# Kernel optimization log

Measured on AMD Instinct MI355X. Metric: run time of the kernel, lower is better.

## Reference

```python
import jax, jax.numpy as jnp
import numpy as np

V, D, N, DK, DV, H, DFF = 32000, 512, 6, 64, 64, 8, 2048
B, S = 8, 512
EPS = 1e-5


def _pe(seq_len, d_model):
    pos = np.arange(seq_len)[:, None].astype(np.float32)
    i = np.arange(0, d_model, 2).astype(np.float32)
    ang = pos / np.power(10000.0, i / d_model)
    pe = np.zeros((seq_len, d_model), dtype=np.float32)
    pe[:, 0::2] = np.sin(ang)
    pe[:, 1::2] = np.cos(ang)
    return jnp.asarray(pe)


def _ln(x, g, b):
    m = jnp.mean(x, axis=-1, keepdims=True)
    v = jnp.mean(jnp.square(x - m), axis=-1, keepdims=True)
    return (x - m) * jax.lax.rsqrt(v + EPS) * g + b


def _mha(xq, xkv, Wq, Wk, Wv, bq, bk, bv, mask):
    # Wq/Wk: [H,D,DK], Wv: [H,D,DV]; mask: [B,Sq,Skv] additive
    q = jnp.einsum('bsd,hdk->bhsk', xq, Wq) + bq[None, :, None, :]
    k = jnp.einsum('bsd,hdk->bhsk', xkv, Wk) + bk[None, :, None, :]
    v = jnp.einsum('bsd,hdk->bhsk', xkv, Wv) + bv[None, :, None, :]
    scores = jnp.einsum('bhqk,bhsk->bhqs', q, k) / jnp.sqrt(jnp.float32(DK))
    scores = scores + mask[:, None, :, :]
    attn = jax.nn.softmax(scores, axis=-1)
    out = jnp.einsum('bhqs,bhsv->bhqv', attn, v)  # [B,H,Sq,DV]
    return out.transpose(0, 2, 1, 3).reshape(xq.shape[0], xq.shape[1], H * DV)


def setup_inputs() -> dict:
    key = jax.random.key(0)
    ks = jax.random.split(key, 24)
    sc = 0.02
    inp = {
        'decoder_input': jax.random.randint(ks[0], (B, S), 0, V),
        'encoder_output': jax.random.normal(ks[1], (B, S, D), dtype=jnp.float32),
        'self_mask': jnp.where(jnp.tril(jnp.ones((S, S), dtype=bool)), 0.0, -1e9)[None].repeat(B, 0).astype(jnp.float32),
        'cross_mask': jnp.zeros((B, S, S), dtype=jnp.float32),
        'emb': jax.random.normal(ks[2], (V, D), dtype=jnp.float32),
        'Wq_s': jax.random.normal(ks[3], (N, H, D, DK)) * sc,
        'Wk_s': jax.random.normal(ks[4], (N, H, D, DK)) * sc,
        'Wv_s': jax.random.normal(ks[5], (N, H, D, DV)) * sc,
        'bq_s': jnp.zeros((N, H, DK)), 'bk_s': jnp.zeros((N, H, DK)), 'bv_s': jnp.zeros((N, H, DV)),
        'Wq_c': jax.random.normal(ks[6], (N, H, D, DK)) * sc,
        'Wk_c': jax.random.normal(ks[7], (N, H, D, DK)) * sc,
        'Wv_c': jax.random.normal(ks[8], (N, H, D, DV)) * sc,
        'bq_c': jnp.zeros((N, H, DK)), 'bk_c': jnp.zeros((N, H, DK)), 'bv_c': jnp.zeros((N, H, DV)),
        'W1': jax.random.normal(ks[9], (N, D, DFF)) * sc,
        'b1': jnp.zeros((N, DFF)),
        'W2': jax.random.normal(ks[10], (N, DFF, D)) * sc,
        'b2': jnp.zeros((N, D)),
        'ln1_g': jnp.ones((N, D)), 'ln1_b': jnp.zeros((N, D)),
        'ln2_g': jnp.ones((N, D)), 'ln2_b': jnp.zeros((N, D)),
    }
    return inp


def reference(decoder_input, encoder_output, self_mask, cross_mask, emb,
              Wq_s, Wk_s, Wv_s, bq_s, bk_s, bv_s,
              Wq_c, Wk_c, Wv_c, bq_c, bk_c, bv_c,
              W1, b1, W2, b2, ln1_g, ln1_b, ln2_g, ln2_b):
    x = emb[decoder_input] + _pe(decoder_input.shape[1], D)[None]
    for l in range(N):
        sa = _mha(x, x, Wq_s[l], Wk_s[l], Wv_s[l], bq_s[l], bk_s[l], bv_s[l], self_mask)
        x = _ln(x + sa, ln1_g[l], ln1_b[l])
        ca = _mha(x, encoder_output, Wq_c[l], Wk_c[l], Wv_c[l], bq_c[l], bk_c[l], bv_c[l], cross_mask)
        x = _ln(x + ca, ln2_g[l], ln2_b[l])
        ff = jax.nn.relu(jnp.einsum('bsd,df->bsf', x, W1[l]) + b1[l])
        ff = jnp.einsum('bsf,fd->bsd', ff, W2[l]) + b2[l]
        # source reuses layer_norm2 for the third norm (layer_norm3 is dead)
        x = _ln(x + ff, ln2_g[l], ln2_b[l])
    return x
```

## Files before the change

kernel.cpp:

```cpp
#include <hip/hip_runtime.h>
#include <hip/hip_bf16.h>
#include <math.h>

#define BB 8
#define SS 512
#define DDIM 512
#define HH 8
#define DFFV 2048
#define NLAYER 6
#define EPSV 1e-5f
#define WQS 0.180336880f

typedef __attribute__((ext_vector_type(8))) short bf16x8;
typedef __attribute__((ext_vector_type(4))) float f32x4;

static __device__ __forceinline__ ushort f2bf(float f) {
  union { float f; unsigned u; } uf; uf.f = f;
  unsigned u = uf.u;
  unsigned r = (u + 0x7fffu + ((u >> 16) & 1u)) >> 16;
  return (ushort)r;
}
static __device__ __forceinline__ float bf2f(ushort h) {
  union { unsigned u; float f; } x;
  x.u = ((unsigned)h) << 16;
  return x.f;
}

static __device__ __forceinline__ void gload_lds16(const void* g, void* l) {
  __builtin_amdgcn_global_load_lds(
      (const __attribute__((address_space(1))) void*)g,
      (__attribute__((address_space(3))) void*)l, 16, 0, 0);
}

__global__ __launch_bounds__(256) void prep_kernel(
    const int* __restrict__ idx, const float* __restrict__ emb,
    const float* __restrict__ enc, const float* __restrict__ bq,
    const float* __restrict__ bk, const float* __restrict__ bv,
    const float* __restrict__ bkc, const float* __restrict__ bvc,
    const float* __restrict__ bqc, ushort* __restrict__ xb,
    ushort* __restrict__ encb, float* __restrict__ qkvb,
    float* __restrict__ ckvb, float* __restrict__ cqb) {
  int gid = blockIdx.x * 256 + threadIdx.x;
  {
    int t0 = gid * 4;
    int bs = t0 >> 9;
    int s = bs & (SS - 1);
    int tok = idx[bs];
    ushort4 o;
    float vv[4];
#pragma unroll
    for (int e = 0; e < 4; e++) {
      int d = (t0 + e) & (DDIM - 1);
      int i2 = d & ~1;
      float ang = (float)s * powf(10000.0f, -((float)i2) / (float)DDIM);
      float pe = (d & 1) ? cosf(ang) : sinf(ang);
      vv[e] = emb[(size_t)tok * DDIM + d] + pe;
    }
    o.x = f2bf(vv[0]); o.y = f2bf(vv[1]); o.z = f2bf(vv[2]); o.w = f2bf(vv[3]);
    *reinterpret_cast<ushort4*>(xb + t0) = o;
  }
  {
    float4 v = reinterpret_cast<const float4*>(enc)[gid];
    ushort4 o;
    o.x = f2bf(v.x); o.y = f2bf(v.y); o.z = f2bf(v.z); o.w = f2bf(v.w);
    reinterpret_cast<ushort4*>(encb)[gid] = o;
  }
  int t = gid;
  if (t < NLAYER * 1536) {
    int l = t / 1536, n = t % 1536;
    float v = n < 512 ? bq[l * 512 + n] * WQS
                      : (n < 1024 ? bk[l * 512 + n - 512] : bv[l * 512 + n - 1024]);
    qkvb[t] = v;
  }
  if (t < NLAYER * 1024) {
    int l = t / 1024, n = t % 1024;
    ckvb[t] = n < 512 ? bkc[l * 512 + n] : bvc[l * 512 + n - 512];
  }
  if (t < NLAYER * 512) cqb[t] = bqc[t] * WQS;
}

__global__ __launch_bounds__(256) void wtrans_kernel(
    const float* __restrict__ in, ushort* __restrict__ out, int R, int C,
    int lgH, size_t zl, float scale) {
  __shared__ float t[32][33];
  int z = blockIdx.z;
  int l = z >> lgH, hh = z & ((1 << lgH) - 1);
  const float* ip = in + (size_t)z * R * C;
  ushort* op = out + (size_t)l * zl + (size_t)hh * R * C;
  int j = threadIdx.x & 31, i0 = threadIdx.x >> 5;
  int r0 = blockIdx.y * 32, c0 = blockIdx.x * 32;
#pragma unroll
  for (int p = 0; p < 4; p++) {
    int r = r0 + i0 + p * 8;
    t[i0 + p * 8][j] = ip[(size_t)r * C + c0 + j];
  }
  __syncthreads();
#pragma unroll
  for (int p = 0; p < 4; p++) {
    int cc = c0 + i0 + p * 8;
    op[(size_t)cc * R + r0 + j] = f2bf(t[j][i0 + p * 8] * scale);
  }
}

__global__ __launch_bounds__(256) void wtrans6_kernel(
    const float* __restrict__ qs, const float* __restrict__ ks,
    const float* __restrict__ vs, const float* __restrict__ qc,
    const float* __restrict__ kc, const float* __restrict__ vc,
    ushort* __restrict__ wqkv, ushort* __restrict__ wqc,
    ushort* __restrict__ wckv) {
  __shared__ float t[32][33];
  int z = blockIdx.z;
  int job = z / 48, zz = z % 48;
  const float* in; ushort* out; size_t zl; float scale;
  switch (job) {
    case 0: in = qs; out = wqkv;           zl = 786432; scale = WQS; break;
    case 1: in = ks; out = wqkv + 262144;  zl = 786432; scale = 1.f; break;
    case 2: in = vs; out = wqkv + 524288;  zl = 786432; scale = 1.f; break;
    case 3: in = qc; out = wqc;            zl = 262144; scale = WQS; break;
    case 4: in = kc; out = wckv;           zl = 524288; scale = 1.f; break;
    default: in = vc; out = wckv + 262144; zl = 524288; scale = 1.f; break;
  }
  int l = zz >> 3, hh = zz & 7;
  const float* ip = in + (size_t)zz * 512 * 64;
  ushort* op = out + (size_t)l * zl + (size_t)hh * 512 * 64;
  int j = threadIdx.x & 31, i0 = threadIdx.x >> 5;
  int r0 = blockIdx.y * 32, c0 = blockIdx.x * 32;
#pragma unroll
  for (int p = 0; p < 4; p++) {
    int r = r0 + i0 + p * 8;
    t[i0 + p * 8][j] = ip[(size_t)r * 64 + c0 + j];
  }
  __syncthreads();
#pragma unroll
  for (int p = 0; p < 4; p++) {
    int cc = c0 + i0 + p * 8;
    op[(size_t)cc * 512 + r0 + j] = f2bf(t[j][i0 + p * 8] * scale);
  }
}

template <int BM, int BN, int RELU, int OUTBF, int NTV, int LGP, int SPLITK,
          int SWZ>
__global__ __launch_bounds__(256) void gemm_mfma(
    const ushort* __restrict__ A, const ushort* __restrict__ Bw,
    const float* __restrict__ bias, float* __restrict__ Cf,
    ushort* __restrict__ Cb, ushort* __restrict__ vt, int M, int N, int K) {
  constexpr int WM = BM / 64;
  constexpr int WN = 4 / WM;
  constexpr int W = BN / WN;
  constexpr int AF = 4;
  constexpr int BF = W / 16;
  constexpr int GA = BM * 8;
  constexpr int GPT = (BM + BN) * 8 / 256;
  __shared__ __align__(16) ushort lds_s[2][(BM + BN) * 64];
  int bn, bm;
  if (SWZ) {
    int nwg = gridDim.x * gridDim.y;
    int wg = blockIdx.y * gridDim.x + blockIdx.x;
    int cpx = nwg >> 3;
    int swz = (wg & 7) * cpx + (wg >> 3);
    bn = (swz % gridDim.x) * BN;
    bm = (swz / gridDim.x) * BM;
  } else {
    bn = blockIdx.x * BN;
    bm = blockIdx.y * BM;
  }
  int kz = (SPLITK > 1) ? blockIdx.z : 0;
  int Keff = K / SPLITK;
  int kbase = kz * Keff;
  int tid = threadIdx.x, lane = tid & 63, w = tid >> 6;
  int wm = w / WN, wn = w % WN;
  int c = lane & 15, g16 = lane >> 4;
  f32x4 acc[AF][BF] = {};

  auto STAGE = [&](int k0, int bufi) {
#pragma unroll
    for (int i = 0; i < GPT; i++) {
      int gidx = i * 256 + tid;
      int gbase = (i * 4 + w) * 64;
      const ushort* src;
      if (gidx < GA) {
        int row = gidx >> 3, dg = gidx & 7;
        src = A + (size_t)(bm + row) * K + kbase + k0 + ((dg ^ (row & 7)) << 3);
      } else {
        int bidx = gidx - GA;
        int row = bidx >> 3, dg = bidx & 7;
        src = Bw + (size_t)(bn + row) * K + kbase + k0 + ((dg ^ (row & 7)) << 3);
      }
      gload_lds16(src, (void*)((char*)(&lds_s[bufi][0]) + gbase * 16));
    }
  };

  int nk = Keff >> 6;
  STAGE(0, 0);
  for (int kt = 0; kt < nk; kt++) {
    int cur = kt & 1;
    if (kt + 1 < nk) {
      STAGE((kt + 1) << 6, cur ^ 1);
      asm volatile("s_waitcnt vmcnt(%0)" ::"n"(GPT) : "memory");
    } else {
      asm volatile("s_waitcnt vmcnt(0)" ::: "memory");
    }
    __builtin_amdgcn_s_barrier();
    __builtin_amdgcn_sched_barrier(0);
    const ushort* Alds = &lds_s[cur][0];
    const ushort* Blds = &lds_s[cur][BM * 64];
#pragma unroll
    for (int ks = 0; ks < 2; ks++) {
      int g = ks * 4 + g16;
      bf16x8 a[AF], b[BF];
#pragma unroll
      for (int i = 0; i < AF; i++) {
        int R = wm * 64 + i * 16 + c;
        a[i] = *(const bf16x8*)(Alds + R * 64 + ((g ^ (R & 7)) << 3));
      }
#pragma unroll
      for (int j = 0; j < BF; j++) {
        int Rb = wn * W + j * 16 + c;
        b[j] = *(const bf16x8*)(Blds + Rb * 64 + ((g ^ (Rb & 7)) << 3));
      }
#pragma unroll
      for (int i = 0; i < AF; i++)
#pragma unroll
        for (int j = 0; j < BF; j++)
          acc[i][j] = __builtin_amdgcn_mfma_f32_16x16x32_bf16(a[i], b[j],
                                                              acc[i][j], 0, 0, 0);
    }
    __builtin_amdgcn_sched_barrier(0);
    __builtin_amdgcn_s_barrier();
  }
  int rb = g16 * 4;
#pragma unroll
  for (int j = 0; j < BF; j++) {
    int col = bn + wn * W + j * 16 + c;
    float bv = (SPLITK > 1 && kz != 0) ? 0.0f : bias[col];
    int cc = LGP ? (col & ((1 << LGP) - 1)) : col;
    int lp = LGP ? (col >> LGP) : 0;
    if (NTV > 0 && cc >= NTV) {
      int hh = (cc - NTV) >> 6, dv = col & 63;
      ushort* vtl = vt + (size_t)lp * 2097152;
#pragma unroll
      for (int i = 0; i < AF; i++) {
        int row = bm + wm * 64 + i * 16 + rb;
        int b_ = row >> 9, s_ = row & 511;
        ushort4 o4;
        o4.x = f2bf(acc[i][j][0] + bv);
        o4.y = f2bf(acc[i][j][1] + bv);
        o4.z = f2bf(acc[i][j][2] + bv);
        o4.w = f2bf(acc[i][j][3] + bv);
        *reinterpret_cast<ushort4*>(
            vtl + ((size_t)(b_ * 8 + hh) * 64 + dv) * 512 + s_) = o4;
      }
    } else {
#pragma unroll
      for (int i = 0; i < AF; i++) {
#pragma unroll
        for (int qq = 0; qq < 4; qq++) {
          int row = bm + wm * 64 + i * 16 + rb + qq;
          float v = acc[i][j][qq] + bv;
          if (RELU) v = fmaxf(v, 0.0f);
          if (OUTBF)
            Cb[(size_t)row * N + col] = f2bf(v);
          else
            Cf[(size_t)kz * M * N + (size_t)row * N + col] = v;
        }
      }
    }
  }
}

template <int MASKED, int NW>
__global__ __launch_bounds__(NW * 64) void attn_mfma(
    const ushort* __restrict__ q, int qstr, const ushort* __restrict__ k,
    int kstr, const ushort* __restrict__ vt, ushort* __restrict__ out) {
  __shared__ __align__(16) char lds[32768 + NW * 2048];
  int h = blockIdx.y, b = blockIdx.z;
  int qc = blockIdx.x;
  if (MASKED && (b & 4)) qc = gridDim.x - 1 - qc;
  int q0 = qc * (NW * 16);
  int tid = threadIdx.x, lane = tid & 63, w = tid >> 6;
  int c = lane & 15, g16 = lane >> 4, rb = g16 * 4;

  bf16x8 qa[2];
#pragma unroll
  for (int ks = 0; ks < 2; ks++)
    qa[ks] = *(const bf16x8*)(q + (size_t)(b * SS + q0 + 16 * w + c) * qstr +
                              h * 64 + ks * 32 + g16 * 8);
  f32x4 o[4] = {};
  float mq = -1e30f, lq = 0.f;

  int nt = MASKED ? (q0 >> 6) + 1 : 8;
  int pbase = 32768 + w * 2048;

  constexpr int GPTK = 512 / (NW * 64);
  bf16x8 rk[GPTK], rv[GPTK];
  const ushort* vbase = vt + ((size_t)(b * 8 + h) * 64) * 512;
  auto LOADT = [&](int kv0) {
#pragma unroll
    for (int i = 0; i < GPTK; i++) {
      int idx = tid + i * (NW * 64);
      int row = idx >> 3, gw = idx & 7;
      rk[i] = *(const bf16x8*)(k + (size_t)(b * SS + kv0 + row) * kstr +
                               h * 64 + gw * 8);
      rv[i] = *(const bf16x8*)(vbase + (size_t)row * 512 + kv0 + gw * 8);
    }
  };
  auto WRT = [&](int bufi) {
    char* p = lds + bufi * 16384;
#pragma unroll
    for (int i = 0; i < GPTK; i++) {
      int idx = tid + i * (NW * 64);
      int row = idx >> 3, gw = idx & 7;
      *(bf16x8*)(p + row * 128 + ((gw ^ (row & 7)) << 4)) = rk[i];
      *(bf16x8*)(p + 8192 + row * 128 + ((gw ^ (row & 7)) << 4)) = rv[i];
    }
  };
  LOADT(0);
  WRT(0);
  for (int t = 0; t < nt; t++) {
    if (t + 1 < nt) LOADT((t + 1) * 64);
    __syncthreads();
    char* kb_ = lds + (t & 1) * 16384;
    char* vb_ = kb_ + 8192;
    f32x4 sp[4] = {};
    __builtin_amdgcn_s_setprio(1);
#pragma unroll
    for (int ks = 0; ks < 2; ks++) {
      int g = ks * 4 + g16;
#pragma unroll
      for (int f = 0; f < 4; f++) {
        int row = f * 16 + c;
        bf16x8 k8 = *(bf16x8*)(kb_ + row * 128 + ((g ^ (row & 7)) << 4));
        sp[f] = __builtin_amdgcn_mfma_f32_16x16x32_bf16(k8, qa[ks], sp[f], 0, 0, 0);
      }
    }
    __builtin_amdgcn_s_setprio(0);
    if (MASKED && t == nt - 1) {
      int ql = 16 * w + c;
#pragma unroll
      for (int f = 0; f < 4; f++)
#pragma unroll
        for (int j = 0; j < 4; j++)
          sp[f][j] += (f * 16 + rb + j) <= ql ? 0.0f : -1e9f;
    }
    float tmax = -1e30f;
#pragma unroll
    for (int f = 0; f < 4; f++)
#pragma unroll
      for (int j = 0; j < 4; j++) tmax = fmaxf(tmax, sp[f][j]);
    tmax = fmaxf(tmax, __shfl_xor(tmax, 16));
    tmax = fmaxf(tmax, __shfl_xor(tmax, 32));
    if (!__all(tmax <= mq + 4.0f)) {
      float mn = fmaxf(mq, tmax);
      float scq = exp2f(mq - mn);
      mq = mn;
      lq *= scq;
      int sb = lane & 48;
#pragma unroll
      for (int j = 0; j < 4; j++) {
        float scj = __shfl(scq, sb | (rb + j));
        o[0][j] *= scj; o[1][j] *= scj; o[2][j] *= scj; o[3][j] *= scj;
      }
    }
    float psum = 0.f;
#pragma unroll
    for (int f = 0; f < 4; f++)
#pragma unroll
      for (int j = 0; j < 4; j++) {
        float pv = exp2f(sp[f][j] - mq);
        sp[f][j] = pv;
        psum += pv;
      }
    psum += __shfl_xor(psum, 16);
    psum += __shfl_xor(psum, 32);
    lq += psum;
#pragma unroll
    for (int f = 0; f < 4; f++) {
      int kv0 = f * 16 + rb;
      ushort4 pk;
      pk.x = f2bf(sp[f][0]); pk.y = f2bf(sp[f][1]);
      pk.z = f2bf(sp[f][2]); pk.w = f2bf(sp[f][3]);
      int gg = kv0 >> 3, off = (kv0 & 7) * 2;
      *(ushort4*)(lds + pbase + c * 128 + ((gg ^ (c & 7)) << 4) + off) = pk;
    }
    __builtin_amdgcn_s_setprio(1);
#pragma unroll
    for (int ks2 = 0; ks2 < 2; ks2++) {
      int g = ks2 * 4 + g16;
      bf16x8 pa = *(bf16x8*)(lds + pbase + c * 128 + ((g ^ (c & 7)) << 4));
#pragma unroll
      for (int f = 0; f < 4; f++) {
        int row = f * 16 + c;
        bf16x8 v8 = *(bf16x8*)(vb_ + row * 128 + ((g ^ (row & 7)) << 4));
        o[f] = __builtin_amdgcn_mfma_f32_16x16x32_bf16(pa, v8, o[f], 0, 0, 0);
      }
    }
    __builtin_amdgcn_s_setprio(0);
    if (t + 1 < nt) WRT((t + 1) & 1);
  }
  float invq = 1.0f / lq;
  int sb = lane & 48;
#pragma unroll
  for (int j = 0; j < 4; j++) {
    float invj = __shfl(invq, sb | (rb + j));
    size_t rowo = (size_t)(b * SS + q0 + 16 * w + rb + j) * 512 + h * 64;
#pragma unroll
    for (int f = 0; f < 4; f++)
      out[rowo + f * 16 + c] = f2bf(o[f][j] * invj);
  }
}

template <int Y2>
__global__ __launch_bounds__(256) void add_ln_kernel(
    ushort* __restrict__ xb, const ushort* __restrict__ yb,
    const float* __restrict__ y0, const float* __restrict__ y1,
    const float* __restrict__ g, const float* __restrict__ bta,
    float* __restrict__ xf) {
  int row = blockIdx.x * 4 + (threadIdx.x >> 6);
  int lane = threadIdx.x & 63;
  int base = row * DDIM + lane * 8;
  bf16x8 xv = *reinterpret_cast<const bf16x8*>(xb + base);
  float v[8];
  if (Y2) {
    float4 a0 = *reinterpret_cast<const float4*>(y0 + base);
    float4 a1 = *reinterpret_cast<const float4*>(y0 + base + 4);
    float4 c0 = *reinterpret_cast<const float4*>(y1 + base);
    float4 c1 = *reinterpret_cast<const float4*>(y1 + base + 4);
    v[0] = bf2f((ushort)xv[0]) + a0.x + c0.x;
    v[1] = bf2f((ushort)xv[1]) + a0.y + c0.y;
    v[2] = bf2f((ushort)xv[2]) + a0.z + c0.z;
    v[3] = bf2f((ushort)xv[3]) + a0.w + c0.w;
    v[4] = bf2f((ushort)xv[4]) + a1.x + c1.x;
    v[5] = bf2f((ushort)xv[5]) + a1.y + c1.y;
    v[6] = bf2f((ushort)xv[6]) + a1.z + c1.z;
    v[7] = bf2f((ushort)xv[7]) + a1.w + c1.w;
  } else {
    bf16x8 yv = *reinterpret_cast<const bf16x8*>(yb + base);
#pragma unroll
    for (int i = 0; i < 8; i++)
      v[i] = bf2f((ushort)xv[i]) + bf2f((ushort)yv[i]);
  }
  float s = 0.f;
#pragma unroll
  for (int i = 0; i < 8; i++) s += v[i];
#pragma unroll
  for (int off = 32; off > 0; off >>= 1) s += __shfl_xor(s, off);
  float mean = s * (1.0f / DDIM);
  float t2 = 0.f;
#pragma unroll
  for (int i = 0; i < 8; i++) {
    v[i] -= mean;
    t2 += v[i] * v[i];
  }
#pragma unroll
  for (int off = 32; off > 0; off >>= 1) t2 += __shfl_xor(t2, off);
  float rs = rsqrtf(t2 * (1.0f / DDIM) + EPSV);
  int cidx = lane * 8;
  float4 g0 = *reinterpret_cast<const float4*>(g + cidx);
  float4 g1 = *reinterpret_cast<const float4*>(g + cidx + 4);
  float4 b0 = *reinterpret_cast<const float4*>(bta + cidx);
  float4 b1 = *reinterpret_cast<const float4*>(bta + cidx + 4);
  float o[8];
  o[0] = v[0] * rs * g0.x + b0.x; o[1] = v[1] * rs * g0.y + b0.y;
  o[2] = v[2] * rs * g0.z + b0.z; o[3] = v[3] * rs * g0.w + b0.w;
  o[4] = v[4] * rs * g1.x + b1.x; o[5] = v[5] * rs * g1.y + b1.y;
  o[6] = v[6] * rs * g1.z + b1.z; o[7] = v[7] * rs * g1.w + b1.w;
  bf16x8 ob;
#pragma unroll
  for (int i = 0; i < 8; i++) ob[i] = (short)f2bf(o[i]);
  *reinterpret_cast<bf16x8*>(xb + base) = ob;
  if (xf) {
    float4 w0 = {o[0], o[1], o[2], o[3]}, w1 = {o[4], o[5], o[6], o[7]};
    *reinterpret_cast<float4*>(xf + base) = w0;
    *reinterpret_cast<float4*>(xf + base + 4) = w1;
  }
}

extern "C" void kernel_launch(void* const* d_in, const int* in_sizes, int n_in,
                              void* d_out, int out_size, void* d_ws,
                              size_t ws_size, hipStream_t stream) {
  const int* dec = (const int*)d_in[0];
  const float* enc = (const float*)d_in[1];
  const float* emb = (const float*)d_in[4];
  const float* Wq_s = (const float*)d_in[5];
  const float* Wk_s = (const float*)d_in[6];
  const float* Wv_s = (const float*)d_in[7];
  const float* bq_s = (const float*)d_in[8];
  const float* bk_s = (const float*)d_in[9];
  const float* bv_s = (const float*)d_in[10];
  const float* Wq_c = (const float*)d_in[11];
  const float* Wk_c = (const float*)d_in[12];
  const float* Wv_c = (const float*)d_in[13];
  const float* bq_c = (const float*)d_in[14];
  const float* bk_c = (const float*)d_in[15];
  const float* bv_c = (const float*)d_in[16];
  const float* W1 = (const float*)d_in[17];
  const float* b1 = (const float*)d_in[18];
  const float* W2 = (const float*)d_in[19];
  const float* b2 = (const float*)d_in[20];
  const float* ln1_g = (const float*)d_in[21];
  const float* ln1_b = (const float*)d_in[22];
  const float* ln2_g = (const float*)d_in[23];
  const float* ln2_b = (const float*)d_in[24];

  char* ws = (char*)d_ws;
  ushort* wqkv = (ushort*)(ws + 0);
  ushort* wqc = (ushort*)(ws + 9437184ull);
  ushort* wckv = (ushort*)(ws + 12582912ull);
  ushort* w1t = (ushort*)(ws + 18874368ull);
  ushort* w2t = (ushort*)(ws + 31457280ull);
  ushort* encb = (ushort*)(ws + 44040192ull);
  ushort* xb = (ushort*)(ws + 48234496ull);
  ushort* tmpb = (ushort*)(ws + 52428800ull);
  float* tmpf = (float*)(ws + 56623104ull);
  ushort* qkvbuf = (ushort*)(ws + 73400320ull);
  ushort* cq = (ushort*)(ws + 73400320ull);
  ushort* ff1b = (ushort*)(ws + 73400320ull);
  ushort* vt = (ushort*)(ws + 85983232ull);
  float* qkvbias = (float*)(ws + 90177536ull);
  float* ckvbias = (float*)(ws + 90214400ull);
  ushort* ckvbuf = (ushort*)(ws + 90238976ull);
  ushort* vtc = (ushort*)(ws + 140570624ull);
  float* cqbias = (float*)(ws + 165736448ull);

  const int M = BB * SS;
  dim3 g256(256);

  prep_kernel<<<dim3(2048), g256, 0, stream>>>(dec, emb, enc, bq_s, bk_s, bv_s,
                                               bk_c, bv_c, bq_c, xb, encb,
                                               qkvbias, ckvbias, cqbias);
  wtrans6_kernel<<<dim3(2, 16, 288), g256, 0, stream>>>(
      Wq_s, Wk_s, Wv_s, Wq_c, Wk_c, Wv_c, wqkv, wqc, wckv);
  wtrans_kernel<<<dim3(64, 16, 6), g256, 0, stream>>>(W1, w1t, 512, 2048, 0,
                                                      1048576ull, 1.0f);
  wtrans_kernel<<<dim3(16, 64, 6), g256, 0, stream>>>(W2, w2t, 2048, 512, 0,
                                                      1048576ull, 1.0f);

  gemm_mfma<128, 128, 0, 1, 512, 10, 1, 0><<<dim3(48, 32), g256, 0, stream>>>(
      encb, wckv, ckvbias, nullptr, ckvbuf, vtc, M, 6144, 512);

  for (int l = 0; l < NLAYER; l++) {
    gemm_mfma<64, 128, 0, 1, 1024, 0, 1, 1><<<dim3(12, 64), g256, 0, stream>>>(
        xb, wqkv + (size_t)l * 786432, qkvbias + l * 1536, nullptr, qkvbuf, vt,
        M, 1536, 512);
    attn_mfma<1, 4><<<dim3(8, 8, 8), g256, 0, stream>>>(
        qkvbuf, 1536, qkvbuf + 512, 1536, vt, tmpb);
    add_ln_kernel<0><<<dim3(M / 4), g256, 0, stream>>>(
        xb, tmpb, nullptr, nullptr, ln1_g + l * 512, ln1_b + l * 512, nullptr);
    gemm_mfma<64, 128, 0, 1, 0, 0, 1, 1><<<dim3(4, 64), g256, 0, stream>>>(
        xb, wqc + (size_t)l * 262144, cqbias + l * 512, nullptr, cq, nullptr,
        M, 512, 512);
    attn_mfma<0, 8><<<dim3(4, 8, 8), dim3(512), 0, stream>>>(
        cq, 512, ckvbuf + l * 1024, 6144, vtc + (size_t)l * 2097152, tmpb);
    add_ln_kernel<0><<<dim3(M / 4), g256, 0, stream>>>(
        xb, tmpb, nullptr, nullptr, ln2_g + l * 512, ln2_b + l * 512, nullptr);
    gemm_mfma<64, 128, 1, 1, 0, 0, 1, 1><<<dim3(16, 64), g256, 0, stream>>>(
        xb, w1t + (size_t)l * 1048576, b1 + l * DFFV, nullptr, ff1b, nullptr,
        M, DFFV, 512);
    gemm_mfma<64, 128, 0, 0, 0, 0, 2, 1><<<dim3(4, 64, 2), g256, 0, stream>>>(
        ff1b, w2t + (size_t)l * 1048576, b2 + l * 512, tmpf, nullptr, nullptr,
        M, 512, DFFV);
    add_ln_kernel<1><<<dim3(M / 4), g256, 0, stream>>>(
        xb, nullptr, tmpf, tmpf + (size_t)M * 512, ln2_g + l * 512,
        ln2_b + l * 512, (l == NLAYER - 1) ? (float*)d_out : nullptr);
  }
}
```

Measured before the change: 621.5 us.

## Fuse cross-attention Q projection into the attention kernel

```diff
diff --git a/kernel.cpp b/kernel.cpp
--- a/kernel.cpp
+++ b/kernel.cpp
@@ -268,10 +268,11 @@
   }
 }
 
-template <int MASKED, int NW>
+template <int MASKED, int NW, int FUSEQ>
 __global__ __launch_bounds__(NW * 64) void attn_mfma(
     const ushort* __restrict__ q, int qstr, const ushort* __restrict__ k,
-    int kstr, const ushort* __restrict__ vt, ushort* __restrict__ out) {
+    int kstr, const ushort* __restrict__ vt, ushort* __restrict__ out,
+    const ushort* __restrict__ wq, const float* __restrict__ qbias) {
   __shared__ __align__(16) char lds[32768 + NW * 2048];
   int h = blockIdx.y, b = blockIdx.z;
   int qc = blockIdx.x;
@@ -279,17 +280,49 @@
   int q0 = qc * (NW * 16);
   int tid = threadIdx.x, lane = tid & 63, w = tid >> 6;
   int c = lane & 15, g16 = lane >> 4, rb = g16 * 4;
+  int pbase = 32768 + w * 2048;
 
   bf16x8 qa[2];
-#pragma unroll
-  for (int ks = 0; ks < 2; ks++)
-    qa[ks] = *(const bf16x8*)(q + (size_t)(b * SS + q0 + 16 * w + c) * qstr +
-                              h * 64 + ks * 32 + g16 * 8);
+  if (!FUSEQ) {
+#pragma unroll
+    for (int ks = 0; ks < 2; ks++)
+      qa[ks] = *(const bf16x8*)(q + (size_t)(b * SS + q0 + 16 * w + c) * qstr +
+                                h * 64 + ks * 32 + g16 * 8);
+  } else {
+    const ushort* wh = wq + h * 32768;
+    const ushort* xrow = q + (size_t)(b * SS + q0 + 16 * w + c) * 512;
+    f32x4 sq[4] = {};
+#pragma unroll
+    for (int kk = 0; kk < 16; kk++) {
+      bf16x8 xf = *(const bf16x8*)(xrow + kk * 32 + g16 * 8);
+#pragma unroll
+      for (int f = 0; f < 4; f++) {
+        bf16x8 wf =
+            *(const bf16x8*)(wh + (size_t)(f * 16 + c) * 512 + kk * 32 + g16 * 8);
+        sq[f] = __builtin_amdgcn_mfma_f32_16x16x32_bf16(wf, xf, sq[f], 0, 0, 0);
+      }
+    }
+    const float* qbh = qbias + h * 64;
+#pragma unroll
+    for (int f = 0; f < 4; f++) {
+      int dk0 = f * 16 + rb;
+      ushort4 qk;
+      qk.x = f2bf(sq[f][0] + qbh[dk0 + 0]);
+      qk.y = f2bf(sq[f][1] + qbh[dk0 + 1]);
+      qk.z = f2bf(sq[f][2] + qbh[dk0 + 2]);
+      qk.w = f2bf(sq[f][3] + qbh[dk0 + 3]);
+      int gg = dk0 >> 3, off = (dk0 & 7) * 2;
+      *(ushort4*)(lds + pbase + c * 128 + ((gg ^ (c & 7)) << 4) + off) = qk;
+    }
+#pragma unroll
+    for (int ks = 0; ks < 2; ks++)
+      qa[ks] =
+          *(bf16x8*)(lds + pbase + c * 128 + (((ks * 4 + g16) ^ (c & 7)) << 4));
+  }
   f32x4 o[4] = {};
   float mq = -1e30f, lq = 0.f;
 
   int nt = MASKED ? (q0 >> 6) + 1 : 8;
-  int pbase = 32768 + w * 2048;
 
   constexpr int GPTK = 512 / (NW * 64);
   bf16x8 rk[GPTK], rv[GPTK];
@@ -513,7 +546,6 @@
   ushort* tmpb = (ushort*)(ws + 52428800ull);
   float* tmpf = (float*)(ws + 56623104ull);
   ushort* qkvbuf = (ushort*)(ws + 73400320ull);
-  ushort* cq = (ushort*)(ws + 73400320ull);
   ushort* ff1b = (ushort*)(ws + 73400320ull);
   ushort* vt = (ushort*)(ws + 85983232ull);
   float* qkvbias = (float*)(ws + 90177536ull);
@@ -542,15 +574,13 @@
     gemm_mfma<64, 128, 0, 1, 1024, 0, 1, 1><<<dim3(12, 64), g256, 0, stream>>>(
         xb, wqkv + (size_t)l * 786432, qkvbias + l * 1536, nullptr, qkvbuf, vt,
         M, 1536, 512);
-    attn_mfma<1, 4><<<dim3(8, 8, 8), g256, 0, stream>>>(
-        qkvbuf, 1536, qkvbuf + 512, 1536, vt, tmpb);
+    attn_mfma<1, 4, 0><<<dim3(8, 8, 8), g256, 0, stream>>>(
+        qkvbuf, 1536, qkvbuf + 512, 1536, vt, tmpb, nullptr, nullptr);
     add_ln_kernel<0><<<dim3(M / 4), g256, 0, stream>>>(
         xb, tmpb, nullptr, nullptr, ln1_g + l * 512, ln1_b + l * 512, nullptr);
-    gemm_mfma<64, 128, 0, 1, 0, 0, 1, 1><<<dim3(4, 64), g256, 0, stream>>>(
-        xb, wqc + (size_t)l * 262144, cqbias + l * 512, nullptr, cq, nullptr,
-        M, 512, 512);
-    attn_mfma<0, 8><<<dim3(4, 8, 8), dim3(512), 0, stream>>>(
-        cq, 512, ckvbuf + l * 1024, 6144, vtc + (size_t)l * 2097152, tmpb);
+    attn_mfma<0, 8, 1><<<dim3(4, 8, 8), dim3(512), 0, stream>>>(
+        xb, 512, ckvbuf + l * 1024, 6144, vtc + (size_t)l * 2097152, tmpb,
+        wqc + (size_t)l * 262144, cqbias + l * 512);
     add_ln_kernel<0><<<dim3(M / 4), g256, 0, stream>>>(
         xb, tmpb, nullptr, nullptr, ln2_g + l * 512, ln2_b + l * 512, nullptr);
     gemm_mfma<64, 128, 1, 1, 0, 0, 1, 1><<<dim3(16, 64), g256, 0, stream>>>(
```

Measured after the change: 674.8 us. +8.6%, slower.
